# Kernel tuning notes

Measured on AMD Instinct MI355X. Metric: run time of the kernel, lower is better.

## Reference

```python
import jax, jax.numpy as jnp
import numpy as np

SAMPLE_RATE = 2048.0
FFTLENGTH = 8.0
NUM_BINS = 16
FFTSIZE = int(FFTLENGTH * SAMPLE_RATE)          # 16384
NUM_FREQS = FFTSIZE // 2 + 1                    # 8193
DF = 1.0 / FFTLENGTH                            # frequency resolution


def setup_inputs() -> dict:
    key = jax.random.key(0)
    k1, k2 = jax.random.split(key)
    template = jax.random.normal(k1, (512, 2, FFTSIZE), dtype=jnp.float32)
    strain = jax.random.normal(k2, (512, 2, FFTSIZE), dtype=jnp.float32)
    return {"template": template, "strain": strain}


def _snr_series(htilde, stilde):
    # snr_frequency_series with psd=None (pre-whitened strain):
    # 4 * df * Re(conj(h) * s)
    return 4.0 * DF * (jnp.conj(htilde) * stilde).real


def reference(template, strain):
    # time -> frequency domain
    htilde = jnp.fft.rfft(template, axis=-1) / SAMPLE_RATE   # [B,C,F] c64
    stilde = jnp.fft.rfft(strain, axis=-1) / SAMPLE_RATE

    # partition_frequencies: cumulative optimal SNR of the template
    cum_h = jnp.cumsum(_snr_series(htilde, htilde), axis=-1)  # [B,C,F]
    total_h = cum_h[..., -1:]                                 # [B,C,1]
    bins = (jnp.arange(NUM_BINS + 1, dtype=cum_h.dtype) / NUM_BINS) * total_h
    # per-row searchsorted (side='right'), vmapped over batch and channel
    edges = jax.vmap(jax.vmap(
        lambda a, v: jnp.searchsorted(a, v, side='right')))(cum_h, bins)
    edges = jnp.clip(edges, 0, cum_h.shape[-1] - 1)           # [B,C,NB+1]
    qtilde = htilde / jnp.sqrt(total_h)                       # normalized template

    # get_snr_per_bin: cumulative matched-filter SNR, gathered at bin edges
    cum_q = jnp.cumsum(_snr_series(qtilde, stilde), axis=-1)  # [B,C,F]
    right = jnp.take_along_axis(cum_q, edges[..., 1:], axis=-1)
    left = jnp.take_along_axis(cum_q, edges[..., :-1], axis=-1)
    snr_per_bin = right - left                                # [B,C,NB]
    total_snr = cum_q[..., -1:]                               # [B,C,1]

    chisq_summand = (snr_per_bin - total_snr / NUM_BINS) ** 2
    chisq = chisq_summand.sum(axis=-1) * (NUM_BINS / (NUM_BINS - 1))
    return chisq                                              # [B,C]
```

## Files before the change

kernel.cpp:

```cpp
#include <hip/hip_runtime.h>
#include <math.h>

#define DPI 3.14159265358979323846

__device__ __forceinline__ float2 cmul(float2 a, float2 b) {
    return make_float2(a.x*b.x - a.y*b.y, a.x*b.y + a.y*b.x);
}
__device__ __forceinline__ float2 cadd(float2 a, float2 b){ return make_float2(a.x+b.x, a.y+b.y); }
__device__ __forceinline__ float2 csub(float2 a, float2 b){ return make_float2(a.x-b.x, a.y-b.y); }
__device__ __forceinline__ float2 mulnj(float2 a){ return make_float2(a.y, -a.x); }

__device__ const float TW32R[16] = {
    1.0f, 0.98078528040323045f, 0.92387953251128676f, 0.83146961230254524f,
    0.70710678118654752f, 0.55557023301960222f, 0.38268343236508977f, 0.19509032201612827f,
    0.0f, -0.19509032201612827f, -0.38268343236508977f, -0.55557023301960222f,
    -0.70710678118654752f, -0.83146961230254524f, -0.92387953251128676f, -0.98078528040323045f };
__device__ const float TW32I[16] = {
    0.0f, -0.19509032201612827f, -0.38268343236508977f, -0.55557023301960222f,
    -0.70710678118654752f, -0.83146961230254524f, -0.92387953251128676f, -0.98078528040323045f,
    -1.0f, -0.98078528040323045f, -0.92387953251128676f, -0.83146961230254524f,
    -0.70710678118654752f, -0.55557023301960222f, -0.38268343236508977f, -0.19509032201612827f };

__device__ const int BR5[32] = {0,16,8,24,4,20,12,28,2,18,10,26,6,22,14,30,
                                1,17,9,25,5,21,13,29,3,19,11,27,7,23,15,31};
__device__ const int BR3[8]  = {0,4,2,6,1,5,3,7};

template<int H>
__device__ __forceinline__ void stage32(float2* y) {
    #pragma unroll
    for (int g = 0; g < 32; g += 2*H) {
        #pragma unroll
        for (int j = 0; j < H; j++) {
            float2 u = y[g+j], v = y[g+j+H];
            y[g+j] = cadd(u, v);
            float2 d = csub(u, v);
            const int m = j * (16 / H);
            y[g+j+H] = (j == 0) ? d : cmul(d, make_float2(TW32R[m], TW32I[m]));
        }
    }
}
__device__ __forceinline__ void fft32(float2* y) {
    stage32<16>(y); stage32<8>(y); stage32<4>(y); stage32<2>(y); stage32<1>(y);
}

__device__ __forceinline__ void fft8(float2* v) {
    const float R2 = 0.70710678118654752f;
    float2 a0=cadd(v[0],v[4]), d0=csub(v[0],v[4]);
    float2 a1=cadd(v[1],v[5]), d1=csub(v[1],v[5]);
    float2 a2=cadd(v[2],v[6]), d2=csub(v[2],v[6]);
    float2 a3=cadd(v[3],v[7]), d3=csub(v[3],v[7]);
    float2 t1 = make_float2(R2*(d1.x+d1.y), R2*(d1.y-d1.x));
    float2 t2 = mulnj(d2);
    float2 t3 = make_float2(R2*(d3.y-d3.x), -R2*(d3.x+d3.y));
    float2 b0=cadd(a0,a2), e0=csub(a0,a2);
    float2 b1=cadd(a1,a3), e1=mulnj(csub(a1,a3));
    float2 c0=cadd(d0,t2), f0=csub(d0,t2);
    float2 c1=cadd(t1,t3), f1=mulnj(csub(t1,t3));
    v[0]=cadd(b0,b1); v[1]=csub(b0,b1);
    v[2]=cadd(e0,e1); v[3]=csub(e0,e1);
    v[4]=cadd(c0,c1); v[5]=csub(c0,c1);
    v[6]=cadd(f0,f1); v[7]=csub(f0,f1);
}

__device__ __forceinline__ void pow16(float2 w, float2* wp) {
    wp[0] = make_float2(1.f, 0.f);
    wp[1] = w;
    wp[2] = cmul(w, w);
    wp[3] = cmul(wp[2], w);
    wp[4] = cmul(wp[2], wp[2]);
    wp[5] = cmul(wp[4], wp[1]);
    wp[6] = cmul(wp[4], wp[2]);
    wp[7] = cmul(wp[4], wp[3]);
    wp[8] = cmul(wp[4], wp[4]);
    wp[9] = cmul(wp[8], wp[1]);
    wp[10] = cmul(wp[8], wp[2]);
    wp[11] = cmul(wp[8], wp[3]);
    wp[12] = cmul(wp[8], wp[4]);
    wp[13] = cmul(wp[8], wp[5]);
    wp[14] = cmul(wp[8], wp[6]);
    wp[15] = cmul(wp[8], wp[7]);
}

static __global__ void init_tw(float2* __restrict__ ws) {
    int t = threadIdx.x;
    if (t < 256) ws[t] = make_float2((float)cos(DPI*t/4096.0), (float)(-sin(DPI*t/4096.0)));
    ws[256 + t] = make_float2((float)cos(DPI*t/512.0), (float)(-sin(DPI*t/512.0)));
    if (t < 16) ws[768 + t] = make_float2((float)cos(DPI*t/8192.0), (float)(-sin(DPI*t/8192.0)));
    if (t < 8)  ws[784 + t] = make_float2((float)cos(DPI*t/128.0),  (float)(-sin(DPI*t/128.0)));
}

__launch_bounds__(512, 2)
static __global__ void chisq_kernel(const float* __restrict__ tmpl,
                                    const float* __restrict__ strn,
                                    const float2* __restrict__ ws,
                                    float* __restrict__ out)
{
    __shared__ float2 Z[16384];
    float* F = reinterpret_cast<float*>(Z);
    int*   I = reinterpret_cast<int*>(Z);

    const int t    = threadIdx.x;
    const int half = t >> 8;
    const int tt   = t & 255;
    const int k1   = tt & 31;
    const int bb   = tt >> 5;
    const int row  = blockIdx.x;
    const float ALPHA = 1.1920928955078125e-7f;

    const float2* twT  = ws;
    const float2* twC  = ws + 256;
    const float2* twI  = ws + 768;
    const float2* twB8 = ws + 784;

    float2* Zh = Z + (half << 13);
    const float* src = (half ? tmpl : strn) + (size_t)row * 16384;

    {
        const float2* x = reinterpret_cast<const float2*>(src);
        float2 y[32];
        #pragma unroll
        for (int n1 = 0; n1 < 32; n1++) y[n1] = x[n1*256 + tt];
        fft32(y);
        float2 wp[16]; pow16(twT[tt], wp);
        float2 w16 = cmul(wp[8], wp[8]);
        #pragma unroll
        for (int p = 0; p < 32; p++) {
            int kk = BR5[p];
            float2 val = y[p];
            if (kk > 0) val = (kk < 16) ? cmul(val, wp[kk]) : cmul(val, cmul(wp[kk-16], w16));
            Zh[(tt << 5) | (kk ^ (tt & 31))] = val;
        }
        __syncthreads();
        #pragma unroll
        for (int a = 0; a < 32; a++) {
            int n2 = 8*a + bb;
            y[a] = Zh[(n2 << 5) | (k1 ^ (n2 & 31))];
        }
        fft32(y);
        float2 wq[16]; pow16(twB8[bb], wq);
        float2 wq16 = cmul(wq[8], wq[8]);
        __syncthreads();
        #pragma unroll
        for (int p = 0; p < 32; p++) {
            int cc = BR5[p];
            float2 val = y[p];
            if (cc > 0) val = (cc < 16) ? cmul(val, wq[cc]) : cmul(val, cmul(wq[cc-16], wq16));
            int r = 8*cc + bb;
            Zh[(r << 5) | (k1 ^ (r & 31))] = val;
        }
        __syncthreads();
        #pragma unroll
        for (int p = 0; p < 4; p++) {
            #pragma unroll
            for (int b2 = 0; b2 < 8; b2++) {
                int r = 8*(4*bb + p) + b2;
                y[p*8 + b2] = Zh[(r << 5) | (k1 ^ (r & 31))];
            }
        }
        __syncthreads();
        #pragma unroll
        for (int p = 0; p < 4; p++) {
            int c = 4*bb + p;
            float2 v8[8];
            #pragma unroll
            for (int b2 = 0; b2 < 8; b2++) v8[b2] = y[p*8 + b2];
            fft8(v8);
            #pragma unroll
            for (int s = 0; s < 8; s++) {
                int d = BR3[s];
                Zh[32*c + 1024*d + (k1 ^ c)] = v8[s];
            }
        }
        __syncthreads();
    }

    float2* ZS = Z;
    float2* ZH = Z + 8192;
    float2 zs0 = ZS[0], zh0 = ZH[0];
    const float s_nyq = zs0.x - zs0.y;
    const float h_nyq = zh0.x - zh0.y;

    float hh[16], hs[16];
    {
        float2 cv = twC[t];
        #pragma unroll
        for (int i = 0; i < 16; i++) {
            int k = (t << 4) + i;
            int m = (8192 - k) & 8191;
            int ak = (k & ~31) | ((k & 31) ^ ((k >> 5) & 31));
            int am = (m & ~31) | ((m & 31) ^ ((m >> 5) & 31));
            float2 As = ZS[ak], Bs = ZS[am];
            float2 Ah = ZH[ak], Bh = ZH[am];
            float2 w = cmul(cv, twI[i]);
            float Er = 0.5f*(As.x + Bs.x), Ei = 0.5f*(As.y - Bs.y);
            float Dr = 0.5f*(As.x - Bs.x), Di = 0.5f*(As.y + Bs.y);
            float sr = Er + w.x*Di + w.y*Dr;
            float si = Ei + w.y*Di - w.x*Dr;
            Er = 0.5f*(Ah.x + Bh.x); Ei = 0.5f*(Ah.y - Bh.y);
            Dr = 0.5f*(Ah.x - Bh.x); Di = 0.5f*(Ah.y + Bh.y);
            float hr = Er + w.x*Di + w.y*Dr;
            float hi = Ei + w.y*Di - w.x*Dr;
            hh[i] = hr*hr + hi*hi;
            hs[i] = hr*sr + hi*si;
        }
    }
    __syncthreads();

    const int SCANW = 16500;
    const int EDG   = 16520;
    const int BINS  = 16544;
    const int TOT   = 16561;

    float run = 0.f;
    #pragma unroll
    for (int i = 0; i < 16; i++) run += ALPHA * hh[i];

    const int lane = t & 63, wid = t >> 6;
    float v = run;
    #pragma unroll
    for (int off = 1; off < 64; off <<= 1) {
        float o = __shfl_up(v, off, 64);
        if (lane >= off) v += o;
    }
    if (lane == 63) F[SCANW + wid] = v;
    __syncthreads();
    float wbase = 0.f;
    #pragma unroll
    for (int w2 = 0; w2 < 7; w2++) if (w2 < wid) wbase += F[SCANW + w2];
    float base = wbase + v - run;

    float cum = base;
    #pragma unroll
    for (int i = 0; i < 16; i++) {
        cum += ALPHA * hh[i];
        int k = (t << 4) + i;
        F[k + (k >> 5)] = cum;
    }
    if (t == 511) F[8448] = cum + ALPHA * h_nyq * h_nyq;
    __syncthreads();

    float total_h = F[8448];
    if (t < 17) {
        float target = (float)t * 0.0625f * total_h;
        int lo = 0, hi = 8193;
        while (lo < hi) {
            int mid = (lo + hi) >> 1;
            float vv = F[mid + (mid >> 5)];
            if (vv <= target) lo = mid + 1; else hi = mid;
        }
        I[EDG + t] = lo < 8192 ? lo : 8192;
    }
    if (t >= 64 && t < 80) F[BINS + (t - 64)] = 0.f;
    if (t == 80) F[TOT] = 0.f;
    __syncthreads();

    int e[17];
    #pragma unroll
    for (int i = 0; i < 17; i++) e[i] = I[EDG + i];

    float invs = 1.0f / sqrtf(total_h);
    float qs   = ALPHA * invs;

    float tot = 0.f, acc = 0.f;
    int   cur = -1;
    #pragma unroll
    for (int i = 0; i < 16; i++) {
        int   k = (t << 4) + i;
        float r = qs * hs[i];
        tot += r;
        int bn = -1;
        #pragma unroll
        for (int j = 0; j < 17; j++) bn += (e[j] < k) ? 1 : 0;
        if (bn != cur) {
            if (cur >= 0) atomicAdd(&F[BINS + cur], acc);
            acc = 0.f;
            cur = bn;
        }
        acc += r;
    }
    if (cur >= 0) atomicAdd(&F[BINS + cur], acc);

    #pragma unroll
    for (int off = 32; off > 0; off >>= 1) tot += __shfl_down(tot, off);
    if ((t & 63) == 0) atomicAdd(&F[TOT], tot);

    if (t == 0) {
        float rn = qs * (h_nyq * s_nyq);
        atomicAdd(&F[TOT], rn);
        int bn = -1;
        #pragma unroll
        for (int j = 0; j < 17; j++) bn += (e[j] < 8192) ? 1 : 0;
        if (bn >= 0) atomicAdd(&F[BINS + bn], rn);
    }
    __syncthreads();

    if (t == 0) {
        float total = F[TOT];
        float mean  = total * 0.0625f;
        float chisq = 0.f;
        #pragma unroll
        for (int j = 0; j < 16; j++) {
            float d = F[BINS + j] - mean;
            chisq += d * d;
        }
        out[row] = chisq * (16.0f / 15.0f);
    }
}

extern "C" void kernel_launch(void* const* d_in, const int* in_sizes, int n_in,
                              void* d_out, int out_size, void* d_ws, size_t ws_size,
                              hipStream_t stream) {
    const float* tmpl = (const float*)d_in[0];
    const float* strn = (const float*)d_in[1];
    float* outp = (float*)d_out;
    float2* ws  = (float2*)d_ws;

    int rows = in_sizes[0] / 16384;

    hipLaunchKernelGGL(init_tw, dim3(1), dim3(512), 0, stream, ws);
    hipLaunchKernelGGL(chisq_kernel, dim3(rows), dim3(512), 0, stream,
                       tmpl, strn, ws, outp);
}
```

Before: 86.02 us.

## Restructure 8192-point FFT as 16x16x32 decomposition over 1024 threads

Replaces the 32x32x8 FFT factorization run on 512 threads (256 per signal) with a 16x16x(2x16) decomposition run on 1024 threads (512 per signal). Each thread now holds 16 complex values instead of 32, which cuts register pressure, and the post-processing, scan and binning loops are rescaled to 8 elements per thread. The twiddle tables and the init kernel are reorganized to match. In exchange there are more threads per block, a single-block-per-CU occupancy target via launch bounds, and extra shared-memory passes for the radix-2 split before the last FFT16.

```diff
diff --git a/kernel.cpp b/kernel.cpp
--- a/kernel.cpp
+++ b/kernel.cpp
@@ -8,7 +8,6 @@
 }
 __device__ __forceinline__ float2 cadd(float2 a, float2 b){ return make_float2(a.x+b.x, a.y+b.y); }
 __device__ __forceinline__ float2 csub(float2 a, float2 b){ return make_float2(a.x-b.x, a.y-b.y); }
-__device__ __forceinline__ float2 mulnj(float2 a){ return make_float2(a.y, -a.x); }
 
 __device__ const float TW32R[16] = {
     1.0f, 0.98078528040323045f, 0.92387953251128676f, 0.83146961230254524f,
@@ -21,14 +20,12 @@
     -1.0f, -0.98078528040323045f, -0.92387953251128676f, -0.83146961230254524f,
     -0.70710678118654752f, -0.55557023301960222f, -0.38268343236508977f, -0.19509032201612827f };
 
-__device__ const int BR5[32] = {0,16,8,24,4,20,12,28,2,18,10,26,6,22,14,30,
-                                1,17,9,25,5,21,13,29,3,19,11,27,7,23,15,31};
-__device__ const int BR3[8]  = {0,4,2,6,1,5,3,7};
+__device__ const int BR4[16] = {0,8,4,12,2,10,6,14,1,9,5,13,3,11,7,15};
 
 template<int H>
-__device__ __forceinline__ void stage32(float2* y) {
-    #pragma unroll
-    for (int g = 0; g < 32; g += 2*H) {
+__device__ __forceinline__ void stage16(float2* y) {
+    #pragma unroll
+    for (int g = 0; g < 16; g += 2*H) {
         #pragma unroll
         for (int j = 0; j < H; j++) {
             float2 u = y[g+j], v = y[g+j+H];
@@ -39,27 +36,8 @@
         }
     }
 }
-__device__ __forceinline__ void fft32(float2* y) {
-    stage32<16>(y); stage32<8>(y); stage32<4>(y); stage32<2>(y); stage32<1>(y);
-}
-
-__device__ __forceinline__ void fft8(float2* v) {
-    const float R2 = 0.70710678118654752f;
-    float2 a0=cadd(v[0],v[4]), d0=csub(v[0],v[4]);
-    float2 a1=cadd(v[1],v[5]), d1=csub(v[1],v[5]);
-    float2 a2=cadd(v[2],v[6]), d2=csub(v[2],v[6]);
-    float2 a3=cadd(v[3],v[7]), d3=csub(v[3],v[7]);
-    float2 t1 = make_float2(R2*(d1.x+d1.y), R2*(d1.y-d1.x));
-    float2 t2 = mulnj(d2);
-    float2 t3 = make_float2(R2*(d3.y-d3.x), -R2*(d3.x+d3.y));
-    float2 b0=cadd(a0,a2), e0=csub(a0,a2);
-    float2 b1=cadd(a1,a3), e1=mulnj(csub(a1,a3));
-    float2 c0=cadd(d0,t2), f0=csub(d0,t2);
-    float2 c1=cadd(t1,t3), f1=mulnj(csub(t1,t3));
-    v[0]=cadd(b0,b1); v[1]=csub(b0,b1);
-    v[2]=cadd(e0,e1); v[3]=csub(e0,e1);
-    v[4]=cadd(c0,c1); v[5]=csub(c0,c1);
-    v[6]=cadd(f0,f1); v[7]=csub(f0,f1);
+__device__ __forceinline__ void fft16(float2* y) {
+    stage16<8>(y); stage16<4>(y); stage16<2>(y); stage16<1>(y);
 }
 
 __device__ __forceinline__ void pow16(float2 w, float2* wp) {
@@ -82,14 +60,22 @@
 }
 
 static __global__ void init_tw(float2* __restrict__ ws) {
-    int t = threadIdx.x;
-    if (t < 256) ws[t] = make_float2((float)cos(DPI*t/4096.0), (float)(-sin(DPI*t/4096.0)));
-    ws[256 + t] = make_float2((float)cos(DPI*t/512.0), (float)(-sin(DPI*t/512.0)));
-    if (t < 16) ws[768 + t] = make_float2((float)cos(DPI*t/8192.0), (float)(-sin(DPI*t/8192.0)));
-    if (t < 8)  ws[784 + t] = make_float2((float)cos(DPI*t/128.0),  (float)(-sin(DPI*t/128.0)));
-}
-
-__launch_bounds__(512, 2)
+    int g = blockIdx.x * 1024 + threadIdx.x;
+    if (g < 512) {
+        ws[g] = make_float2((float)cos(DPI*g/4096.0), (float)(-sin(DPI*g/4096.0)));
+    } else if (g < 544) {
+        int j = g - 512;
+        ws[g] = make_float2((float)cos(DPI*j/256.0), (float)(-sin(DPI*j/256.0)));
+    } else if (g < 1568) {
+        int q = g - 544;
+        ws[g] = make_float2((float)cos(DPI*q/1024.0), (float)(-sin(DPI*q/1024.0)));
+    } else if (g < 1576) {
+        int i = g - 1568;
+        ws[g] = make_float2((float)cos(DPI*i/8192.0), (float)(-sin(DPI*i/8192.0)));
+    }
+}
+
+__launch_bounds__(1024)
 static __global__ void chisq_kernel(const float* __restrict__ tmpl,
                                     const float* __restrict__ strn,
                                     const float2* __restrict__ ws,
@@ -100,76 +86,78 @@
     int*   I = reinterpret_cast<int*>(Z);
 
     const int t    = threadIdx.x;
-    const int half = t >> 8;
-    const int tt   = t & 255;
-    const int k1   = tt & 31;
-    const int bb   = tt >> 5;
+    const int half = t >> 9;
+    const int u    = t & 511;
     const int row  = blockIdx.x;
     const float ALPHA = 1.1920928955078125e-7f;
 
-    const float2* twT  = ws;
-    const float2* twC  = ws + 256;
-    const float2* twI  = ws + 768;
-    const float2* twB8 = ws + 784;
+    const float2* tw8192 = ws;
+    const float2* tw512  = ws + 512;
+    const float2* twC    = ws + 544;
+    const float2* twI    = ws + 1568;
 
     float2* Zh = Z + (half << 13);
     const float* src = (half ? tmpl : strn) + (size_t)row * 16384;
 
     {
         const float2* x = reinterpret_cast<const float2*>(src);
-        float2 y[32];
-        #pragma unroll
-        for (int n1 = 0; n1 < 32; n1++) y[n1] = x[n1*256 + tt];
-        fft32(y);
-        float2 wp[16]; pow16(twT[tt], wp);
-        float2 w16 = cmul(wp[8], wp[8]);
-        #pragma unroll
-        for (int p = 0; p < 32; p++) {
-            int kk = BR5[p];
-            float2 val = y[p];
-            if (kk > 0) val = (kk < 16) ? cmul(val, wp[kk]) : cmul(val, cmul(wp[kk-16], w16));
-            Zh[(tt << 5) | (kk ^ (tt & 31))] = val;
-        }
-        __syncthreads();
-        #pragma unroll
-        for (int a = 0; a < 32; a++) {
-            int n2 = 8*a + bb;
-            y[a] = Zh[(n2 << 5) | (k1 ^ (n2 & 31))];
-        }
-        fft32(y);
-        float2 wq[16]; pow16(twB8[bb], wq);
-        float2 wq16 = cmul(wq[8], wq[8]);
-        __syncthreads();
-        #pragma unroll
-        for (int p = 0; p < 32; p++) {
-            int cc = BR5[p];
-            float2 val = y[p];
-            if (cc > 0) val = (cc < 16) ? cmul(val, wq[cc]) : cmul(val, cmul(wq[cc-16], wq16));
-            int r = 8*cc + bb;
-            Zh[(r << 5) | (k1 ^ (r & 31))] = val;
-        }
-        __syncthreads();
-        #pragma unroll
-        for (int p = 0; p < 4; p++) {
+        float2 y[16];
+
+        #pragma unroll
+        for (int n1 = 0; n1 < 16; n1++) y[n1] = x[n1*512 + u];
+        fft16(y);
+        {
+            float2 wp[16]; pow16(tw8192[u], wp);
             #pragma unroll
-            for (int b2 = 0; b2 < 8; b2++) {
-                int r = 8*(4*bb + p) + b2;
-                y[p*8 + b2] = Zh[(r << 5) | (k1 ^ (r & 31))];
+            for (int p = 0; p < 16; p++) {
+                int k1 = BR4[p];
+                float2 val = y[p];
+                if (k1 > 0) val = cmul(val, wp[k1]);
+                Zh[(u << 4) | (k1 ^ (u & 15))] = val;
             }
         }
         __syncthreads();
-        #pragma unroll
-        for (int p = 0; p < 4; p++) {
-            int c = 4*bb + p;
-            float2 v8[8];
+
+        const int k1s = u >> 5, js = u & 31;
+        #pragma unroll
+        for (int n2 = 0; n2 < 16; n2++)
+            y[n2] = Zh[((n2*32 + js) << 4) | (k1s ^ (js & 15))];
+        __syncthreads();
+        fft16(y);
+        {
+            float2 wq[16]; pow16(tw512[js], wq);
             #pragma unroll
-            for (int b2 = 0; b2 < 8; b2++) v8[b2] = y[p*8 + b2];
-            fft8(v8);
+            for (int p = 0; p < 16; p++) {
+                int k2 = BR4[p];
+                float2 val = y[p];
+                if (k2 > 0) val = cmul(val, wq[k2]);
+                Zh[(k1s << 9) + (k2 << 5) + (js ^ k2)] = val;
+            }
+        }
+        __syncthreads();
+
+        const int f = u >> 8, k1t = (u >> 4) & 15, k2t = u & 15;
+        const int base = (k1t << 9) + (k2t << 5);
+        float2 A[16], B[16];
+        #pragma unroll
+        for (int j2 = 0; j2 < 16; j2++) A[j2] = Zh[base + (j2 ^ k2t)];
+        #pragma unroll
+        for (int j2 = 0; j2 < 16; j2++) B[j2] = Zh[base + (j2 ^ k2t) + 16];
+        if (f == 0) {
             #pragma unroll
-            for (int s = 0; s < 8; s++) {
-                int d = BR3[s];
-                Zh[32*c + 1024*d + (k1 ^ c)] = v8[s];
-            }
+            for (int j2 = 0; j2 < 16; j2++) y[j2] = cadd(A[j2], B[j2]);
+        } else {
+            #pragma unroll
+            for (int j2 = 0; j2 < 16; j2++)
+                y[j2] = cmul(csub(A[j2], B[j2]), make_float2(TW32R[j2], TW32I[j2]));
+        }
+        __syncthreads();
+        fft16(y);
+        #pragma unroll
+        for (int p = 0; p < 16; p++) {
+            int s2 = BR4[p];
+            int k = k1t + (k2t << 4) + (f << 8) + (s2 << 9);
+            Zh[(k & ~31) | ((k & 31) ^ ((k >> 5) & 31))] = y[p];
         }
         __syncthreads();
     }
@@ -180,12 +168,12 @@
     const float s_nyq = zs0.x - zs0.y;
     const float h_nyq = zh0.x - zh0.y;
 
-    float hh[16], hs[16];
+    float hh[8], hs[8];
     {
         float2 cv = twC[t];
         #pragma unroll
-        for (int i = 0; i < 16; i++) {
-            int k = (t << 4) + i;
+        for (int i = 0; i < 8; i++) {
+            int k = (t << 3) + i;
             int m = (8192 - k) & 8191;
             int ak = (k & ~31) | ((k & 31) ^ ((k >> 5) & 31));
             int am = (m & ~31) | ((m & 31) ^ ((m >> 5) & 31));
@@ -213,7 +201,7 @@
 
     float run = 0.f;
     #pragma unroll
-    for (int i = 0; i < 16; i++) run += ALPHA * hh[i];
+    for (int i = 0; i < 8; i++) run += ALPHA * hh[i];
 
     const int lane = t & 63, wid = t >> 6;
     float v = run;
@@ -226,17 +214,17 @@
     __syncthreads();
     float wbase = 0.f;
     #pragma unroll
-    for (int w2 = 0; w2 < 7; w2++) if (w2 < wid) wbase += F[SCANW + w2];
+    for (int w2 = 0; w2 < 15; w2++) if (w2 < wid) wbase += F[SCANW + w2];
     float base = wbase + v - run;
 
     float cum = base;
     #pragma unroll
-    for (int i = 0; i < 16; i++) {
+    for (int i = 0; i < 8; i++) {
         cum += ALPHA * hh[i];
-        int k = (t << 4) + i;
+        int k = (t << 3) + i;
         F[k + (k >> 5)] = cum;
     }
-    if (t == 511) F[8448] = cum + ALPHA * h_nyq * h_nyq;
+    if (t == 1023) F[8448] = cum + ALPHA * h_nyq * h_nyq;
     __syncthreads();
 
     float total_h = F[8448];
@@ -264,8 +252,8 @@
     float tot = 0.f, acc = 0.f;
     int   cur = -1;
     #pragma unroll
-    for (int i = 0; i < 16; i++) {
-        int   k = (t << 4) + i;
+    for (int i = 0; i < 8; i++) {
+        int   k = (t << 3) + i;
         float r = qs * hs[i];
         tot += r;
         int bn = -1;
@@ -317,7 +305,7 @@
 
     int rows = in_sizes[0] / 16384;
 
-    hipLaunchKernelGGL(init_tw, dim3(1), dim3(512), 0, stream, ws);
-    hipLaunchKernelGGL(chisq_kernel, dim3(rows), dim3(512), 0, stream,
+    hipLaunchKernelGGL(init_tw, dim3(2), dim3(1024), 0, stream, ws);
+    hipLaunchKernelGGL(chisq_kernel, dim3(rows), dim3(1024), 0, stream,
                        tmpl, strn, ws, outp);
 }
```

Result: faster. 82.56 us (-4.0%).
